# Optimization experiments

Hardware: AMD Instinct MI355X
Metric: run time of the kernel (lower is better)

## Reference

```python
import jax, jax.numpy as jnp
import numpy as np

N_NODES = 50000


def _sage_conv(x, src, dst, Wl, bl, Wr):
    # PyG SAGEConv (mean aggr): out = lin_l(mean_{j in N(i)} x_j) + lin_r(x_i)
    msgs = x[src]                                              # [E, F]
    agg = jax.ops.segment_sum(msgs, dst, num_segments=N_NODES)  # [N, F]
    cnt = jax.ops.segment_sum(jnp.ones((dst.shape[0],), x.dtype), dst,
                              num_segments=N_NODES)
    mean = agg / jnp.maximum(cnt, 1.0)[:, None]
    return mean @ Wl + bl + x @ Wr


def setup_inputs() -> dict:
    key = jax.random.key(0)
    ks = jax.random.split(key, 12)
    in_c, hid_c, out_c = 128, 128, 64
    E, P = 800000, 200000
    s = lambda k, shp: jax.random.normal(k, shp, dtype=jnp.float32) * (1.0 / np.sqrt(shp[0]))
    return {
        "x": jax.random.normal(ks[0], (N_NODES, in_c), dtype=jnp.float32),
        "edge_index": jax.random.randint(ks[1], (2, E), 0, N_NODES),
        "edge_pairs": jax.random.randint(ks[2], (2, P), 0, N_NODES),
        "W1l": s(ks[3], (in_c, hid_c)),
        "b1": jnp.zeros((hid_c,), jnp.float32),
        "W1r": s(ks[4], (in_c, hid_c)),
        "W2l": s(ks[5], (hid_c, out_c)),
        "b2": jnp.zeros((out_c,), jnp.float32),
        "W2r": s(ks[6], (hid_c, out_c)),
        "Wlin": s(ks[7], (2 * out_c, 1)),
        "blin": jnp.zeros((1,), jnp.float32),
    }


def reference(x, edge_index, edge_pairs, W1l, b1, W1r, W2l, b2, W2r, Wlin, blin):
    src, dst = edge_index[0], edge_index[1]
    h = jax.nn.relu(_sage_conv(x, src, dst, W1l, b1, W1r))
    z = _sage_conv(h, src, dst, W2l, b2, W2r)                 # [N, out_c]
    ps, pd = edge_pairs[0], edge_pairs[1]
    hcat = jnp.concatenate([z[ps], z[pd]], axis=1)            # [P, 2*out_c]
    logits = hcat @ Wlin + blin                               # [P, 1]
    return jax.nn.sigmoid(logits).reshape(-1)
```

## Files before the change

### kernel.cpp

```cpp
#include <hip/hip_runtime.h>
#include <math.h>


typedef __attribute__((ext_vector_type(8))) short bf16x8;
typedef __attribute__((ext_vector_type(4))) float f32x4;
typedef unsigned int uint32;
typedef unsigned short ushort16;

#define MAXBUCK 784
#define NHB 512

__device__ __forceinline__ ushort16 f2bf(float f) {
    uint32 u = __float_as_uint(f);
    uint32 r = u + 0x7FFFu + ((u >> 16) & 1u);
    return (ushort16)(r >> 16);
}


__global__ __launch_bounds__(256)
void prep_kernel(const float* __restrict__ x, uint32* __restrict__ xh, long long n4,
                 const float* __restrict__ W1l, const float* __restrict__ W1r,
                 ushort16* __restrict__ W1t,
                 const float* __restrict__ W2l, const float* __restrict__ W2r,
                 const float* __restrict__ Wlin, const float* __restrict__ b2,
                 float* __restrict__ fw, float* __restrict__ fc,
                 const int* __restrict__ dst, int* __restrict__ hcnt, int E,
                 int nbx, int nbw1) {
    __shared__ int lh[MAXBUCK];
    int b = blockIdx.x;
    int t = threadIdx.x;
    if (b < nbx) {
        long long i = (long long)b * 256 + t;
        if (i < n4) {
            float4 v = ((const float4*)x)[i];
            uint2 o;
            o.x = (uint32)f2bf(v.x) | ((uint32)f2bf(v.y) << 16);
            o.y = (uint32)f2bf(v.z) | ((uint32)f2bf(v.w) << 16);
            ((uint2*)xh)[i] = o;
        }
    } else if (b < nbx + nbw1) {
        int idx = (b - nbx) * 256 + t;
        int n = idx >> 8, k = idx & 255;
        float v = (k < 128) ? W1l[k * 128 + n] : W1r[(k - 128) * 128 + n];
        W1t[n * 256 + k] = f2bf(v);
    } else if (b == nbx + nbw1) {
        if (t < 128) {
            float a = 0.f, c = 0.f;
            for (int l = 0; l < 64; ++l) {
                float w = W2l[t * 64 + l];
                a += w * Wlin[l];
                c += w * Wlin[64 + l];
            }
            fw[t] = a; fw[128 + t] = c;
        } else {
            int k = t - 128;
            float a = 0.f, c = 0.f;
            for (int l = 0; l < 64; ++l) {
                float w = W2r[k * 64 + l];
                a += w * Wlin[l];
                c += w * Wlin[64 + l];
            }
            fw[256 + k] = a; fw[384 + k] = c;
        }
        if (t == 0) { float s = 0.f; for (int l = 0; l < 64; ++l) s += b2[l] * Wlin[l];      fc[0] = s; }
        if (t == 1) { float s = 0.f; for (int l = 0; l < 64; ++l) s += b2[l] * Wlin[64 + l]; fc[1] = s; }
    } else {
        int hb = b - nbx - nbw1 - 1;
        for (int i = t; i < MAXBUCK; i += 256) lh[i] = 0;
        __syncthreads();
        int per = (E + NHB - 1) / NHB;
        int e0 = hb * per, e1 = min(e0 + per, E);
        for (int e = e0 + t; e < e1; e += 256) atomicAdd(&lh[dst[e] >> 6], 1);
        __syncthreads();
        for (int i = t; i < MAXBUCK; i += 256)
            hcnt[hb * MAXBUCK + i] = lh[i];
    }
}


__global__ __launch_bounds__(256)
void offs_kernel(const int* __restrict__ hcnt, int* __restrict__ boff,
                 int* __restrict__ tot) {
    int k = blockIdx.x * 4 + (threadIdx.x >> 6);
    int lane = threadIdx.x & 63;
    if (k >= MAXBUCK) return;
    int carry = 0;
    #pragma unroll
    for (int c = 0; c < NHB / 64; ++c) {
        int hb = c * 64 + lane;
        int v = hcnt[hb * MAXBUCK + k];
        int s = v;
        #pragma unroll
        for (int off = 1; off < 64; off <<= 1) {
            int u = __shfl_up(s, off, 64);
            if (lane >= off) s += u;
        }
        boff[hb * MAXBUCK + k] = carry + s - v;
        carry += __shfl(s, 63, 64);
    }
    if (lane == 0) tot[k] = carry;
}


__global__ void bucket_scan_kernel(const int* __restrict__ tot,
                                   int* __restrict__ bbase, int nbuck) {
    __shared__ int part[256];
    int t = threadIdx.x;
    int lo = t * 4;
    int hi = min(lo + 4, nbuck);
    int loc[4];
    int s = 0;
    for (int i = lo; i < hi; ++i) { loc[i - lo] = tot[i]; s += loc[i - lo]; }
    part[t] = s;
    __syncthreads();
    for (int off = 1; off < 256; off <<= 1) {
        int v = (t >= off) ? part[t - off] : 0;
        __syncthreads();
        part[t] += v;
        __syncthreads();
    }
    int run = (t == 0) ? 0 : part[t - 1];
    for (int i = lo; i < hi; ++i) { bbase[i] = run; run += loc[i - lo]; }
    if (t == 255) bbase[nbuck] = part[255];
}


__global__ __launch_bounds__(256)
void scatter_kernel(const int* __restrict__ src, const int* __restrict__ dst,
                    const int* __restrict__ bbase, const int* __restrict__ boff,
                    uint32* __restrict__ recs, int E) {
    __shared__ int lh[MAXBUCK];
    __shared__ int lb[MAXBUCK];
    int t = threadIdx.x;
    int hb = blockIdx.x;
    int per = (E + NHB - 1) / NHB;
    int e0 = hb * per, e1 = min(e0 + per, E);
    for (int i = t; i < MAXBUCK; i += 256) {
        lh[i] = 0;
        lb[i] = bbase[i] + boff[hb * MAXBUCK + i];
    }
    __syncthreads();
    for (int e = e0 + t; e < e1; e += 256) {
        int d = dst[e];
        int b = d >> 6;
        int r = atomicAdd(&lh[b], 1);
        recs[lb[b] + r] = (uint32)src[e] | ((uint32)(d & 63) << 16);
    }
}


__global__ __launch_bounds__(256)
void sort_kernel(const uint32* __restrict__ recs, const int* __restrict__ bbase,
                 int* __restrict__ rowptr, ushort16* __restrict__ esrc,
                 int N, int E) {
    __shared__ int lh[64];
    int b = blockIdx.x;
    int t = threadIdx.x;
    int s0 = bbase[b], s1 = bbase[b + 1];
    if (t < 64) lh[t] = 0;
    __syncthreads();
    for (int i = s0 + t; i < s1; i += 256)
        atomicAdd(&lh[recs[i] >> 16], 1);
    __syncthreads();
    if (t < 64) {
        int v = lh[t];
        int incl = v;
        #pragma unroll
        for (int off = 1; off < 64; off <<= 1) {
            int u = __shfl_up(incl, off, 64);
            if (t >= off) incl += u;
        }
        int excl = incl - v;
        int node = b * 64 + t;
        if (node < N) rowptr[node] = s0 + excl;
        lh[t] = excl;
    }
    __syncthreads();
    for (int i = s0 + t; i < s1; i += 256) {
        uint32 r = recs[i];
        int pos = atomicAdd(&lh[r >> 16], 1);
        esrc[s0 + pos] = (ushort16)(r & 0xFFFFu);
    }
    if (b == 0 && t == 0) rowptr[N] = E;
}


__global__ __launch_bounds__(256)
void agg_mean_x_kernel(const uint32* __restrict__ xh,
                       const int* __restrict__ rowptr,
                       const ushort16* __restrict__ esrc,
                       uint32* __restrict__ meanh, int N) {
    int node = blockIdx.x * 4 + (threadIdx.x >> 6);
    int lane = threadIdx.x & 63;
    if (node >= N) return;
    int s0 = rowptr[node], s1 = rowptr[node + 1];
    int q = lane >> 4;
    int w = lane & 15;
    if (s0 == s1) {
        if (q == 0) ((uint4*)meanh)[(size_t)node * 16 + w] = make_uint4(0u, 0u, 0u, 0u);
        return;
    }
    float acc[8] = {};
    for (int k = s0; k < s1; k += 16) {
        int e[4]; int idx[4]; float msk[4];
        #pragma unroll
        for (int j = 0; j < 4; ++j) {
            e[j] = k + q * 4 + j;
            int valid = e[j] < s1;
            idx[j] = esrc[valid ? e[j] : s0];
            msk[j] = valid ? 1.f : 0.f;
        }
        #pragma unroll
        for (int j = 0; j < 4; ++j) {
            uint4 v = ((const uint4*)xh)[(size_t)idx[j] * 16 + w];
            acc[0] += __uint_as_float(v.x << 16) * msk[j];
            acc[1] += __uint_as_float(v.x & 0xFFFF0000u) * msk[j];
            acc[2] += __uint_as_float(v.y << 16) * msk[j];
            acc[3] += __uint_as_float(v.y & 0xFFFF0000u) * msk[j];
            acc[4] += __uint_as_float(v.z << 16) * msk[j];
            acc[5] += __uint_as_float(v.z & 0xFFFF0000u) * msk[j];
            acc[6] += __uint_as_float(v.w << 16) * msk[j];
            acc[7] += __uint_as_float(v.w & 0xFFFF0000u) * msk[j];
        }
    }
    #pragma unroll
    for (int i = 0; i < 8; ++i) {
        acc[i] += __shfl_xor(acc[i], 16, 64);
        acc[i] += __shfl_xor(acc[i], 32, 64);
    }
    if (q == 0) {
        float inv = 1.0f / (float)(s1 - s0);
        uint4 o;
        o.x = (uint32)f2bf(acc[0] * inv) | ((uint32)f2bf(acc[1] * inv) << 16);
        o.y = (uint32)f2bf(acc[2] * inv) | ((uint32)f2bf(acc[3] * inv) << 16);
        o.z = (uint32)f2bf(acc[4] * inv) | ((uint32)f2bf(acc[5] * inv) << 16);
        o.w = (uint32)f2bf(acc[6] * inv) | ((uint32)f2bf(acc[7] * inv) << 16);
        ((uint4*)meanh)[(size_t)node * 16 + w] = o;
    }
}


__global__ __launch_bounds__(256)
void gemm1_mfma_kernel(const ushort16* __restrict__ meanh,
                       const ushort16* __restrict__ xh,
                       const ushort16* __restrict__ W1t,
                       const float* __restrict__ b1,
                       const float* __restrict__ fw,
                       float2* __restrict__ pab, float2* __restrict__ quv, int N) {
    int wave = threadIdx.x >> 6;
    int lane = threadIdx.x & 63;
    int m = lane & 15;
    int quad = lane >> 4;
    int row0 = blockIdx.x * 64 + wave * 16;
    int arow = row0 + m; if (arow > N - 1) arow = N - 1;
    f32x4 acc[8];
    #pragma unroll
    for (int c = 0; c < 8; ++c) acc[c] = (f32x4){0.f, 0.f, 0.f, 0.f};
    #pragma unroll
    for (int ks = 0; ks < 8; ++ks) {
        int k0 = ks * 32;
        const ushort16* Ab = (ks < 4) ? meanh : xh;
        bf16x8 a = *(const bf16x8*)(Ab + (size_t)arow * 128 + (k0 & 127) + quad * 8);
        #pragma unroll
        for (int c = 0; c < 8; ++c) {
            bf16x8 b = *(const bf16x8*)(W1t + (size_t)(c * 16 + m) * 256 + k0 + quad * 8);
            acc[c] = __builtin_amdgcn_mfma_f32_16x16x32_bf16(a, b, acc[c], 0, 0, 0);
        }
    }
    float da[4] = {}, dc[4] = {}, db[4] = {}, dd[4] = {};
    #pragma unroll
    for (int c = 0; c < 8; ++c) {
        int col = c * 16 + m;
        float bias = b1[col];
        float wa = fw[col], wc = fw[128 + col], wb = fw[256 + col], wd = fw[384 + col];
        #pragma unroll
        for (int r = 0; r < 4; ++r) {
            float v = fmaxf(acc[c][r] + bias, 0.f);
            da[r] += v * wa; dc[r] += v * wc; db[r] += v * wb; dd[r] += v * wd;
        }
    }
    #pragma unroll
    for (int r = 0; r < 4; ++r) {
        #pragma unroll
        for (int msk = 1; msk < 16; msk <<= 1) {
            da[r] += __shfl_xor(da[r], msk, 64);
            dc[r] += __shfl_xor(dc[r], msk, 64);
            db[r] += __shfl_xor(db[r], msk, 64);
            dd[r] += __shfl_xor(dd[r], msk, 64);
        }
    }
    if (m == 0) {
        #pragma unroll
        for (int r = 0; r < 4; ++r) {
            int grow = row0 + quad * 4 + r;
            if (grow < N) {
                pab[grow] = make_float2(da[r], dc[r]);
                quv[grow] = make_float2(db[r], dd[r]);
            }
        }
    }
}


__global__ __launch_bounds__(256)
void agg_link_kernel(const float2* __restrict__ pab,
                     const float2* __restrict__ quv,
                     const int* __restrict__ rowptr,
                     const ushort16* __restrict__ esrc,
                     const float* __restrict__ fc,
                     float* __restrict__ za, float* __restrict__ zb, int N) {
    int gi = blockIdx.x * blockDim.x + threadIdx.x;
    int i = gi >> 2;
    int q = gi & 3;
    if (i >= N) return;
    int s0 = rowptr[i], s1 = rowptr[i + 1];
    float a0 = 0.f, c0 = 0.f, a1 = 0.f, c1 = 0.f;
    for (int k = s0 + q; k < s1; k += 8) {
        int kB = k + 4;
        int vB = kB < s1;
        int idxA = esrc[k];
        int idxB = esrc[vB ? kB : k];
        float2 pA = pab[idxA];
        float2 pB = pab[idxB];
        float mB = vB ? 1.f : 0.f;
        a0 += pA.x; c0 += pA.y;
        a1 += pB.x * mB; c1 += pB.y * mB;
    }
    float spa = a0 + a1, spc = c0 + c1;
    spa += __shfl_xor(spa, 1, 64); spa += __shfl_xor(spa, 2, 64);
    spc += __shfl_xor(spc, 1, 64); spc += __shfl_xor(spc, 2, 64);
    if (q == 0) {
        float inv = (s1 > s0) ? 1.0f / (float)(s1 - s0) : 0.f;
        float2 qv = quv[i];
        za[i] = spa * inv + qv.x + fc[0];
        zb[i] = spc * inv + qv.y + fc[1];
    }
}


__global__ void link_kernel(const float* __restrict__ za, const float* __restrict__ zb,
                            const int* __restrict__ ps, const int* __restrict__ pd,
                            const float* __restrict__ blin,
                            float* __restrict__ out, int P) {
    int p = blockIdx.x * blockDim.x + threadIdx.x;
    if (p >= P) return;
    float logit = za[ps[p]] + zb[pd[p]] + blin[0];
    out[p] = 1.0f / (1.0f + expf(-logit));
}


extern "C" void kernel_launch(void* const* d_in, const int* in_sizes, int n_in,
                              void* d_out, int out_size, void* d_ws, size_t ws_size,
                              hipStream_t stream) {
    const float* x          = (const float*)d_in[0];
    const int*   edge_index = (const int*)d_in[1];
    const int*   edge_pairs = (const int*)d_in[2];
    const float* W1l        = (const float*)d_in[3];
    const float* b1         = (const float*)d_in[4];
    const float* W1r        = (const float*)d_in[5];
    const float* W2l        = (const float*)d_in[6];
    const float* b2         = (const float*)d_in[7];
    const float* W2r        = (const float*)d_in[8];
    const float* Wlin       = (const float*)d_in[9];
    const float* blin       = (const float*)d_in[10];
    float* out = (float*)d_out;

    const int N = in_sizes[0] / 128;
    const int E = in_sizes[1] / 2;
    const int P = in_sizes[2] / 2;
    const int NBUCK = (N + 63) >> 6;

    const int* src = edge_index;
    const int* dst = edge_index + E;
    const int* ps  = edge_pairs;
    const int* pd  = edge_pairs + P;

    ushort16* xh    = (ushort16*)d_ws;
    ushort16* meanh = xh + (size_t)N * 128;
    ushort16* W1t   = meanh + (size_t)N * 128;
    float* fw      = (float*)(W1t + 128 * 256);
    float* fc      = fw + 512;
    float2* pab    = (float2*)(fc + 4);
    float2* quv    = pab + N;
    float* za      = (float*)(quv + N);
    float* zb      = za + N;
    int* bbase     = (int*)(zb + N);
    int* tot       = bbase + (MAXBUCK + 16);
    int* hcnt      = tot + MAXBUCK;
    int* boff      = hcnt + NHB * MAXBUCK;
    int* rowptr    = boff + NHB * MAXBUCK;
    uint32* recs   = (uint32*)(rowptr + N + 16);
    ushort16* esrc = (ushort16*)(recs + E);

    const long long n4 = (long long)N * 128 / 4;
    const int nbx  = (int)((n4 + 255) / 256);
    const int nbw1 = 128;

    prep_kernel<<<nbx + nbw1 + 1 + NHB, 256, 0, stream>>>(
        x, (uint32*)xh, n4, W1l, W1r, W1t, W2l, W2r, Wlin, b2, fw, fc,
        dst, hcnt, E, nbx, nbw1);

    offs_kernel<<<MAXBUCK / 4, 256, 0, stream>>>(hcnt, boff, tot);
    bucket_scan_kernel<<<1, 256, 0, stream>>>(tot, bbase, NBUCK);
    scatter_kernel<<<NHB, 256, 0, stream>>>(src, dst, bbase, boff, recs, E);
    sort_kernel<<<NBUCK, 256, 0, stream>>>(recs, bbase, rowptr, esrc, N, E);

    agg_mean_x_kernel<<<(N + 3) / 4, 256, 0, stream>>>((const uint32*)xh, rowptr, esrc,
                                                       (uint32*)meanh, N);
    gemm1_mfma_kernel<<<(N + 63) / 64, 256, 0, stream>>>(meanh, xh, W1t, b1, fw,
                                                         pab, quv, N);

    agg_link_kernel<<<(4 * N + 255) / 256, 256, 0, stream>>>(pab, quv, rowptr, esrc, fc,
                                                             za, zb, N);

    link_kernel<<<(P + 255) / 256, 256, 0, stream>>>(za, zb, ps, pd, blin, out, P);
}
```

Baseline: 195.3 us.

## Fuse per-bucket sort with first-layer mean aggregation; double rows per GEMM wave

Merges the bucket counting sort and the mean aggregation of x into one 1024-thread kernel per 64-node bucket. Sorted source indices stay in shared memory (up to CAP entries) so the gather reads them locally, and one kernel launch plus a global round trip of esrc are removed. Each bucket's 64 nodes are now handled by only 16 waves in a single block, so per-block parallelism changes and load balance may suffer. Separately, the first GEMM processes 32 rows per wave with two accumulator sets, reusing each W1 fragment across two MFMAs at the cost of more registers.

```diff
diff --git a/kernel.cpp b/kernel.cpp
--- a/kernel.cpp
+++ b/kernel.cpp
@@ -9,6 +9,7 @@
 
 #define MAXBUCK 784
 #define NHB 512
+#define CAP 2048
 
 __device__ __forceinline__ ushort16 f2bf(float f) {
     uint32 u = __float_as_uint(f);
@@ -149,17 +150,20 @@
 }
 
 
-__global__ __launch_bounds__(256)
-void sort_kernel(const uint32* __restrict__ recs, const int* __restrict__ bbase,
-                 int* __restrict__ rowptr, ushort16* __restrict__ esrc,
-                 int N, int E) {
+__global__ __launch_bounds__(1024)
+void sortagg_kernel(const uint32* __restrict__ xh,
+                    const uint32* __restrict__ recs, const int* __restrict__ bbase,
+                    int* __restrict__ rowptr, ushort16* __restrict__ esrc_g,
+                    uint32* __restrict__ meanh, int N, int E) {
     __shared__ int lh[64];
+    __shared__ int st_[64];
+    __shared__ unsigned short es[CAP];
     int b = blockIdx.x;
     int t = threadIdx.x;
     int s0 = bbase[b], s1 = bbase[b + 1];
     if (t < 64) lh[t] = 0;
     __syncthreads();
-    for (int i = s0 + t; i < s1; i += 256)
+    for (int i = s0 + t; i < s1; i += 1024)
         atomicAdd(&lh[recs[i] >> 16], 1);
     __syncthreads();
     if (t < 64) {
@@ -173,69 +177,71 @@
         int excl = incl - v;
         int node = b * 64 + t;
         if (node < N) rowptr[node] = s0 + excl;
+        st_[t] = excl;
         lh[t] = excl;
     }
-    __syncthreads();
-    for (int i = s0 + t; i < s1; i += 256) {
+    if (b == 0 && t == 0) rowptr[N] = E;
+    __syncthreads();
+    for (int i = s0 + t; i < s1; i += 1024) {
         uint32 r = recs[i];
         int pos = atomicAdd(&lh[r >> 16], 1);
-        esrc[s0 + pos] = (ushort16)(r & 0xFFFFu);
-    }
-    if (b == 0 && t == 0) rowptr[N] = E;
-}
-
-
-__global__ __launch_bounds__(256)
-void agg_mean_x_kernel(const uint32* __restrict__ xh,
-                       const int* __restrict__ rowptr,
-                       const ushort16* __restrict__ esrc,
-                       uint32* __restrict__ meanh, int N) {
-    int node = blockIdx.x * 4 + (threadIdx.x >> 6);
-    int lane = threadIdx.x & 63;
-    if (node >= N) return;
-    int s0 = rowptr[node], s1 = rowptr[node + 1];
+        unsigned short sv = (unsigned short)(r & 0xFFFFu);
+        if (pos < CAP) es[pos] = sv;
+        ((unsigned short*)esrc_g)[s0 + pos] = sv;
+    }
+    __syncthreads();
+
+    int wave = t >> 6, lane = t & 63;
     int q = lane >> 4;
     int w = lane & 15;
-    if (s0 == s1) {
-        if (q == 0) ((uint4*)meanh)[(size_t)node * 16 + w] = make_uint4(0u, 0u, 0u, 0u);
-        return;
-    }
-    float acc[8] = {};
-    for (int k = s0; k < s1; k += 16) {
-        int e[4]; int idx[4]; float msk[4];
-        #pragma unroll
-        for (int j = 0; j < 4; ++j) {
-            e[j] = k + q * 4 + j;
-            int valid = e[j] < s1;
-            idx[j] = esrc[valid ? e[j] : s0];
-            msk[j] = valid ? 1.f : 0.f;
-        }
-        #pragma unroll
-        for (int j = 0; j < 4; ++j) {
-            uint4 v = ((const uint4*)xh)[(size_t)idx[j] * 16 + w];
-            acc[0] += __uint_as_float(v.x << 16) * msk[j];
-            acc[1] += __uint_as_float(v.x & 0xFFFF0000u) * msk[j];
-            acc[2] += __uint_as_float(v.y << 16) * msk[j];
-            acc[3] += __uint_as_float(v.y & 0xFFFF0000u) * msk[j];
-            acc[4] += __uint_as_float(v.z << 16) * msk[j];
-            acc[5] += __uint_as_float(v.z & 0xFFFF0000u) * msk[j];
-            acc[6] += __uint_as_float(v.w << 16) * msk[j];
-            acc[7] += __uint_as_float(v.w & 0xFFFF0000u) * msk[j];
-        }
-    }
-    #pragma unroll
-    for (int i = 0; i < 8; ++i) {
-        acc[i] += __shfl_xor(acc[i], 16, 64);
-        acc[i] += __shfl_xor(acc[i], 32, 64);
-    }
-    if (q == 0) {
-        float inv = 1.0f / (float)(s1 - s0);
-        uint4 o;
-        o.x = (uint32)f2bf(acc[0] * inv) | ((uint32)f2bf(acc[1] * inv) << 16);
-        o.y = (uint32)f2bf(acc[2] * inv) | ((uint32)f2bf(acc[3] * inv) << 16);
-        o.z = (uint32)f2bf(acc[4] * inv) | ((uint32)f2bf(acc[5] * inv) << 16);
-        o.w = (uint32)f2bf(acc[6] * inv) | ((uint32)f2bf(acc[7] * inv) << 16);
-        ((uint4*)meanh)[(size_t)node * 16 + w] = o;
+    for (int rr = 0; rr < 4; ++rr) {
+        int n = wave * 4 + rr;
+        int node = b * 64 + n;
+        if (node >= N) break;
+        int e0 = st_[n], e1 = lh[n];
+        if (e0 == e1) {
+            if (q == 0) ((uint4*)meanh)[(size_t)node * 16 + w] = make_uint4(0u, 0u, 0u, 0u);
+            continue;
+        }
+        float acc[8] = {};
+        for (int k = e0; k < e1; k += 16) {
+            int idx[4]; float msk[4];
+            #pragma unroll
+            for (int j = 0; j < 4; ++j) {
+                int e = k + q * 4 + j;
+                int valid = e < e1;
+                int ksel = valid ? e : e0;
+                idx[j] = (ksel < CAP) ? es[ksel]
+                                      : ((const unsigned short*)esrc_g)[s0 + ksel];
+                msk[j] = valid ? 1.f : 0.f;
+            }
+            #pragma unroll
+            for (int j = 0; j < 4; ++j) {
+                uint4 v = ((const uint4*)xh)[(size_t)idx[j] * 16 + w];
+                acc[0] += __uint_as_float(v.x << 16) * msk[j];
+                acc[1] += __uint_as_float(v.x & 0xFFFF0000u) * msk[j];
+                acc[2] += __uint_as_float(v.y << 16) * msk[j];
+                acc[3] += __uint_as_float(v.y & 0xFFFF0000u) * msk[j];
+                acc[4] += __uint_as_float(v.z << 16) * msk[j];
+                acc[5] += __uint_as_float(v.z & 0xFFFF0000u) * msk[j];
+                acc[6] += __uint_as_float(v.w << 16) * msk[j];
+                acc[7] += __uint_as_float(v.w & 0xFFFF0000u) * msk[j];
+            }
+        }
+        #pragma unroll
+        for (int i = 0; i < 8; ++i) {
+            acc[i] += __shfl_xor(acc[i], 16, 64);
+            acc[i] += __shfl_xor(acc[i], 32, 64);
+        }
+        if (q == 0) {
+            float inv = 1.0f / (float)(e1 - e0);
+            uint4 o;
+            o.x = (uint32)f2bf(acc[0] * inv) | ((uint32)f2bf(acc[1] * inv) << 16);
+            o.y = (uint32)f2bf(acc[2] * inv) | ((uint32)f2bf(acc[3] * inv) << 16);
+            o.z = (uint32)f2bf(acc[4] * inv) | ((uint32)f2bf(acc[5] * inv) << 16);
+            o.w = (uint32)f2bf(acc[6] * inv) | ((uint32)f2bf(acc[7] * inv) << 16);
+            ((uint4*)meanh)[(size_t)node * 16 + w] = o;
+        }
     }
 }
 
@@ -251,51 +257,66 @@
     int lane = threadIdx.x & 63;
     int m = lane & 15;
     int quad = lane >> 4;
-    int row0 = blockIdx.x * 64 + wave * 16;
-    int arow = row0 + m; if (arow > N - 1) arow = N - 1;
-    f32x4 acc[8];
+    int row0 = blockIdx.x * 128 + wave * 32;
+    int ar0 = row0 + m;      if (ar0 > N - 1) ar0 = N - 1;
+    int ar1 = row0 + 16 + m; if (ar1 > N - 1) ar1 = N - 1;
+    f32x4 acc[2][8];
     #pragma unroll
-    for (int c = 0; c < 8; ++c) acc[c] = (f32x4){0.f, 0.f, 0.f, 0.f};
+    for (int h = 0; h < 2; ++h)
+        #pragma unroll
+        for (int c = 0; c < 8; ++c) acc[h][c] = (f32x4){0.f, 0.f, 0.f, 0.f};
     #pragma unroll
     for (int ks = 0; ks < 8; ++ks) {
         int k0 = ks * 32;
         const ushort16* Ab = (ks < 4) ? meanh : xh;
-        bf16x8 a = *(const bf16x8*)(Ab + (size_t)arow * 128 + (k0 & 127) + quad * 8);
+        bf16x8 a0 = *(const bf16x8*)(Ab + (size_t)ar0 * 128 + (k0 & 127) + quad * 8);
+        bf16x8 a1 = *(const bf16x8*)(Ab + (size_t)ar1 * 128 + (k0 & 127) + quad * 8);
         #pragma unroll
         for (int c = 0; c < 8; ++c) {
-            bf16x8 b = *(const bf16x8*)(W1t + (size_t)(c * 16 + m) * 256 + k0 + quad * 8);
-            acc[c] = __builtin_amdgcn_mfma_f32_16x16x32_bf16(a, b, acc[c], 0, 0, 0);
-        }
-    }
-    float da[4] = {}, dc[4] = {}, db[4] = {}, dd[4] = {};
+            bf16x8 bfr = *(const bf16x8*)(W1t + (size_t)(c * 16 + m) * 256 + k0 + quad * 8);
+            acc[0][c] = __builtin_amdgcn_mfma_f32_16x16x32_bf16(a0, bfr, acc[0][c], 0, 0, 0);
+            acc[1][c] = __builtin_amdgcn_mfma_f32_16x16x32_bf16(a1, bfr, acc[1][c], 0, 0, 0);
+        }
+    }
+    float da[2][4] = {}, dc[2][4] = {}, db[2][4] = {}, dd[2][4] = {};
     #pragma unroll
     for (int c = 0; c < 8; ++c) {
         int col = c * 16 + m;
         float bias = b1[col];
         float wa = fw[col], wc = fw[128 + col], wb = fw[256 + col], wd = fw[384 + col];
         #pragma unroll
+        for (int h = 0; h < 2; ++h) {
+            #pragma unroll
+            for (int r = 0; r < 4; ++r) {
+                float v = fmaxf(acc[h][c][r] + bias, 0.f);
+                da[h][r] += v * wa; dc[h][r] += v * wc;
+                db[h][r] += v * wb; dd[h][r] += v * wd;
+            }
+        }
+    }
+    #pragma unroll
+    for (int h = 0; h < 2; ++h) {
+        #pragma unroll
         for (int r = 0; r < 4; ++r) {
-            float v = fmaxf(acc[c][r] + bias, 0.f);
-            da[r] += v * wa; dc[r] += v * wc; db[r] += v * wb; dd[r] += v * wd;
-        }
-    }
-    #pragma unroll
-    for (int r = 0; r < 4; ++r) {
-        #pragma unroll
-        for (int msk = 1; msk < 16; msk <<= 1) {
-            da[r] += __shfl_xor(da[r], msk, 64);
-            dc[r] += __shfl_xor(dc[r], msk, 64);
-            db[r] += __shfl_xor(db[r], msk, 64);
-            dd[r] += __shfl_xor(dd[r], msk, 64);
+            #pragma unroll
+            for (int msk = 1; msk < 16; msk <<= 1) {
+                da[h][r] += __shfl_xor(da[h][r], msk, 64);
+                dc[h][r] += __shfl_xor(dc[h][r], msk, 64);
+                db[h][r] += __shfl_xor(db[h][r], msk, 64);
+                dd[h][r] += __shfl_xor(dd[h][r], msk, 64);
+            }
         }
     }
     if (m == 0) {
         #pragma unroll
-        for (int r = 0; r < 4; ++r) {
-            int grow = row0 + quad * 4 + r;
-            if (grow < N) {
-                pab[grow] = make_float2(da[r], dc[r]);
-                quv[grow] = make_float2(db[r], dd[r]);
+        for (int h = 0; h < 2; ++h) {
+            #pragma unroll
+            for (int r = 0; r < 4; ++r) {
+                int grow = row0 + h * 16 + quad * 4 + r;
+                if (grow < N) {
+                    pab[grow] = make_float2(da[h][r], dc[h][r]);
+                    quv[grow] = make_float2(db[h][r], dd[h][r]);
+                }
             }
         }
     }
@@ -403,12 +424,12 @@
     offs_kernel<<<MAXBUCK / 4, 256, 0, stream>>>(hcnt, boff, tot);
     bucket_scan_kernel<<<1, 256, 0, stream>>>(tot, bbase, NBUCK);
     scatter_kernel<<<NHB, 256, 0, stream>>>(src, dst, bbase, boff, recs, E);
-    sort_kernel<<<NBUCK, 256, 0, stream>>>(recs, bbase, rowptr, esrc, N, E);
-
-    agg_mean_x_kernel<<<(N + 3) / 4, 256, 0, stream>>>((const uint32*)xh, rowptr, esrc,
-                                                       (uint32*)meanh, N);
-    gemm1_mfma_kernel<<<(N + 63) / 64, 256, 0, stream>>>(meanh, xh, W1t, b1, fw,
-                                                         pab, quv, N);
+
+    sortagg_kernel<<<NBUCK, 1024, 0, stream>>>((const uint32*)xh, recs, bbase,
+                                               rowptr, esrc, (uint32*)meanh, N, E);
+
+    gemm1_mfma_kernel<<<(N + 127) / 128, 256, 0, stream>>>(meanh, xh, W1t, b1, fw,
+                                                           pab, quv, N);
 
     agg_link_kernel<<<(4 * N + 255) / 256, 256, 0, stream>>>(pab, quv, rowptr, esrc, fc,
                                                              za, zb, N);
```

New measurement: 184.5 us. 5.5% less time.
